# Optimization experiments

Hardware: AMD Instinct MI355X
Metric: run time of the kernel (lower is better)

## Reference

```python
import jax, jax.numpy as jnp
import numpy as np

N, E = 100000, 1000000
IN_DIM, HID, OUT_DIM, TAU_DIM, MAX_REC = 128, 64, 64, 8, 5


def setup_inputs() -> dict:
    key = jax.random.key(0)
    ks = jax.random.split(key, 16)
    s = 0.05
    return {
        "x": jax.random.normal(ks[0], (N, IN_DIM), dtype=jnp.float32),
        "edge_index": jax.random.randint(ks[1], (2, E), 0, N, dtype=jnp.int64),
        "W_in": jax.random.normal(ks[2], (HID, IN_DIM), dtype=jnp.float32) * s,
        "b_in": jnp.zeros((HID,), jnp.float32),
        "W_t1": jax.random.normal(ks[3], (HID, IN_DIM), dtype=jnp.float32) * s,
        "b_t1": jnp.zeros((HID,), jnp.float32),
        "W_t2": jax.random.normal(ks[4], (TAU_DIM, HID), dtype=jnp.float32) * s,
        "b_t2": jnp.zeros((TAU_DIM,), jnp.float32),
        "W_ih": jax.random.normal(ks[5], (3 * HID, HID), dtype=jnp.float32) * s,
        "b_ih": jnp.zeros((3 * HID,), jnp.float32),
        "W_hh": jax.random.normal(ks[6], (3 * HID, HID), dtype=jnp.float32) * s,
        "b_hh": jnp.zeros((3 * HID,), jnp.float32),
        "W_out": jax.random.normal(ks[7], (OUT_DIM, HID), dtype=jnp.float32) * s,
        "b_out": jnp.zeros((OUT_DIM,), jnp.float32),
    }


def _gru_cell(inp, h, W_ih, b_ih, W_hh, b_hh):
    # torch.nn.GRUCell math
    gi = inp @ W_ih.T + b_ih  # [N, 3H]
    gh = h @ W_hh.T + b_hh    # [N, 3H]
    i_r, i_z, i_n = jnp.split(gi, 3, axis=-1)
    h_r, h_z, h_n = jnp.split(gh, 3, axis=-1)
    r = jax.nn.sigmoid(i_r + h_r)
    z = jax.nn.sigmoid(i_z + h_z)
    n = jnp.tanh(i_n + r * h_n)
    return (1.0 - z) * n + z * h


def reference(x, edge_index, W_in, b_in, W_t1, b_t1, W_t2, b_t2,
              W_ih, b_ih, W_hh, b_hh, W_out, b_out):
    row, col = edge_index[0], edge_index[1]
    h = jax.nn.relu(x @ W_in.T + b_in)  # [N, H]
    tau = jax.nn.sigmoid(jax.nn.relu(x @ W_t1.T + b_t1) @ W_t2.T + b_t2)
    tau = jnp.mean(tau, axis=-1, keepdims=True)  # [N, 1]
    for _ in range(MAX_REC):
        d1 = jnp.abs(h[row] - h[col])           # gather + diff, [E, H]
        weighted = d1 * tau[row]                # [E, H]
        agg = jax.ops.segment_sum(weighted, row, num_segments=h.shape[0])
        h = _gru_cell(agg, h, W_ih, b_ih, W_hh, b_hh)
    return h @ W_out.T + b_out
```

## Files before the change

### kernel.cpp

```cpp
#include <hip/hip_runtime.h>

#define HID 64
#define IN_DIM 128
#define TAU_DIM 8
#define SCAN_B 1024

#define KDIM 128
#define NT 64
#define JOUT 256
#define WS_STRIDE 20

typedef short bf16x8 __attribute__((ext_vector_type(8)));
typedef float f32x4 __attribute__((ext_vector_type(4)));

__device__ __forceinline__ unsigned short f2bf(float f) {
    union { float f; unsigned u; } v; v.f = f;
    unsigned r = v.u + 0x7FFF + ((v.u >> 16) & 1);
    return (unsigned short)(r >> 16);
}


__global__ void zero_int_kernel(int* __restrict__ p, int n) {
    int i = blockIdx.x * blockDim.x + threadIdx.x;
    if (i < n) p[i] = 0;
}

__global__ void count_deg_kernel(const int* __restrict__ row, int* __restrict__ deg,
                                 int e, int n) {
    int i = blockIdx.x * blockDim.x + threadIdx.x;
    if (i < e) {
        int r = row[i];
        if ((unsigned)r < (unsigned)n) atomicAdd(&deg[r], 1);
    }
}

__global__ void block_sum_kernel(const int* __restrict__ deg, int* __restrict__ blk, int n) {
    __shared__ int s[SCAN_B];
    int i = blockIdx.x * SCAN_B + threadIdx.x;
    s[threadIdx.x] = (i < n) ? deg[i] : 0;
    __syncthreads();
    for (int off = SCAN_B / 2; off > 0; off >>= 1) {
        if (threadIdx.x < off) s[threadIdx.x] += s[threadIdx.x + off];
        __syncthreads();
    }
    if (threadIdx.x == 0) blk[blockIdx.x] = s[0];
}

__global__ void scan_blk_kernel(int* __restrict__ blk, int nb) {
    __shared__ int s[SCAN_B];
    int v = (threadIdx.x < nb) ? blk[threadIdx.x] : 0;
    s[threadIdx.x] = v;
    __syncthreads();
    for (int off = 1; off < SCAN_B; off <<= 1) {
        int t = (threadIdx.x >= off) ? s[threadIdx.x - off] : 0;
        __syncthreads();
        s[threadIdx.x] += t;
        __syncthreads();
    }
    if (threadIdx.x < nb) blk[threadIdx.x] = s[threadIdx.x] - v;
}

__global__ void scan_final_kernel(const int* __restrict__ deg, const int* __restrict__ blk,
                                  int* __restrict__ row_start, int* __restrict__ cursor, int n) {
    __shared__ int s[SCAN_B];
    int i = blockIdx.x * SCAN_B + threadIdx.x;
    int v = (i < n) ? deg[i] : 0;
    s[threadIdx.x] = v;
    __syncthreads();
    for (int off = 1; off < SCAN_B; off <<= 1) {
        int t = (threadIdx.x >= off) ? s[threadIdx.x - off] : 0;
        __syncthreads();
        s[threadIdx.x] += t;
        __syncthreads();
    }
    if (i < n) {
        int excl = s[threadIdx.x] - v + blk[blockIdx.x];
        row_start[i] = excl;
        cursor[i]    = excl;
    }
}

__global__ void fill_csr_kernel(const int* __restrict__ row, const int* __restrict__ col,
                                int* __restrict__ cursor, int* __restrict__ cols,
                                int e, int n) {
    int i = blockIdx.x * blockDim.x + threadIdx.x;
    if (i < e) {
        int r = row[i];
        if ((unsigned)r < (unsigned)n) {
            int c = col[i];
            if ((unsigned)c >= (unsigned)n) c = 0;
            int p = atomicAdd(&cursor[r], 1);
            cols[p] = c;
        }
    }
}


__global__ void prep_all_kernel(
    const float* __restrict__ W_ih, const float* __restrict__ W_hh,
    const float* __restrict__ b_ih, const float* __restrict__ b_hh,
    const float* __restrict__ W_in, const float* __restrict__ b_in,
    const float* __restrict__ W_t1, const float* __restrict__ b_t1,
    const float* __restrict__ W_out,
    unsigned short* __restrict__ W2bf, float* __restrict__ B2,
    unsigned short* __restrict__ W1bf, float* __restrict__ B1,
    float* __restrict__ Wop) {
    int j = threadIdx.x;
    {
        float b;
        if (j < 128)      b = b_ih[j] + b_hh[j];
        else if (j < 192) b = b_ih[j];
        else              b = b_hh[j - 64];
        B2[j] = b;
        for (int k = 0; k < KDIM; k++) {
            float v;
            if (j < 128)      v = (k < 64) ? W_ih[j * 64 + k] : W_hh[j * 64 + (k - 64)];
            else if (j < 192) v = (k < 64) ? W_ih[j * 64 + k] : 0.f;
            else              v = (k >= 64) ? W_hh[(j - 64) * 64 + (k - 64)] : 0.f;
            W2bf[(size_t)j * KDIM + k] = f2bf(v);
        }
    }
    if (j < 128) {
        B1[j] = (j < 64) ? b_in[j] : b_t1[j - 64];
        const float* src = (j < 64) ? (W_in + (size_t)j * IN_DIM)
                                    : (W_t1 + (size_t)(j - 64) * IN_DIM);
        for (int k = 0; k < IN_DIM; k++)
            W1bf[(size_t)j * IN_DIM + k] = f2bf(src[k]);
    }
    if (j < 64) {
        for (int k = 0; k < HID; k++)
            Wop[(size_t)(k >> 4) * (64 * 16) + j * 16 + (k & 15)] = W_out[(size_t)j * HID + k];
    }
}


__global__ __launch_bounds__(256) void init_mfma_kernel(
    const float* __restrict__ x, const unsigned short* __restrict__ W1bf,
    const float* __restrict__ B1,
    const float* __restrict__ W_t2, const float* __restrict__ b_t2,
    float* __restrict__ X1, float* __restrict__ tau, int n) {
    __shared__ float t1s[NT * 65];

    const int t    = threadIdx.x;
    const int lane = t & 63;
    const int wave = t >> 6;
    const int col  = lane & 15;
    const int ksel = lane >> 4;
    const int nodebase = blockIdx.x * NT + wave * 16;

    bf16x8 afrag[4];
    {
        const int anode = nodebase + col;
#pragma unroll
        for (int kc = 0; kc < 4; kc++) {
            bf16x8 a;
            if (anode < n) {
                const float* p = x + (size_t)anode * IN_DIM + kc * 32 + ksel * 8;
                float4 lo = *(const float4*)p;
                float4 hi = *(const float4*)(p + 4);
                a[0] = (short)f2bf(lo.x); a[1] = (short)f2bf(lo.y);
                a[2] = (short)f2bf(lo.z); a[3] = (short)f2bf(lo.w);
                a[4] = (short)f2bf(hi.x); a[5] = (short)f2bf(hi.y);
                a[6] = (short)f2bf(hi.z); a[7] = (short)f2bf(hi.w);
            } else {
                a[0] = 0; a[1] = 0; a[2] = 0; a[3] = 0;
                a[4] = 0; a[5] = 0; a[6] = 0; a[7] = 0;
            }
            afrag[kc] = a;
        }
    }

#pragma unroll 1
    for (int i = 0; i < 8; i++) {
        float b = B1[i * 16 + col];
        f32x4 c; c[0] = b; c[1] = b; c[2] = b; c[3] = b;
#pragma unroll
        for (int kc = 0; kc < 4; kc++) {
            bf16x8 bf = *(const bf16x8*)(W1bf
                + (size_t)(i * 16 + col) * IN_DIM + kc * 32 + ksel * 8);
            c = __builtin_amdgcn_mfma_f32_16x16x32_bf16(afrag[kc], bf, c, 0, 0, 0);
        }
#pragma unroll
        for (int r = 0; r < 4; r++) {
            int node = nodebase + ksel * 4 + r;
            float v = fmaxf(c[r], 0.f);
            if (i < 4) {
                if (node < n) X1[(size_t)node * KDIM + 64 + i * 16 + col] = v;
            } else {
                t1s[(wave * 16 + ksel * 4 + r) * 65 + (i - 4) * 16 + col] = v;
            }
        }
    }
    __syncthreads();

    if (t < NT) {
        int node = blockIdx.x * NT + t;
        if (node < n) {
            float tsum = 0.f;
#pragma unroll 1
            for (int m = 0; m < TAU_DIM; m++) {
                float a = b_t2[m];
                const float* wr = W_t2 + (size_t)m * HID;
#pragma unroll
                for (int k = 0; k < HID; k++) a += wr[k] * t1s[t * 65 + k];
                tsum += 1.f / (1.f + expf(-a));
            }
            tau[node] = tsum * (1.f / TAU_DIM);
        }
    }
}


__global__ __launch_bounds__(256) void aggregate_kernel(
    float* __restrict__ X1, const float* __restrict__ tau,
    const int* __restrict__ row_start, const int* __restrict__ deg,
    const int* __restrict__ cols, int n, int hoff, int aoff) {
    int t = blockIdx.x * blockDim.x + threadIdx.x;
    int v = t >> 4;
    if (v >= n) return;
    int c4 = (t & 15) * 4;

    float4 hv = *(const float4*)(X1 + (size_t)v * KDIM + hoff + c4);
    float4 s0 = make_float4(0.f, 0.f, 0.f, 0.f);
    float4 s1 = make_float4(0.f, 0.f, 0.f, 0.f);
    int st = row_start[v];
    int d  = deg[v];
    int i = 0;
    for (; i + 1 < d; i += 2) {
        int c0 = cols[st + i];
        int c1 = cols[st + i + 1];
        float4 hc0 = *(const float4*)(X1 + (size_t)c0 * KDIM + hoff + c4);
        float4 hc1 = *(const float4*)(X1 + (size_t)c1 * KDIM + hoff + c4);
        s0.x += fabsf(hv.x - hc0.x);
        s0.y += fabsf(hv.y - hc0.y);
        s0.z += fabsf(hv.z - hc0.z);
        s0.w += fabsf(hv.w - hc0.w);
        s1.x += fabsf(hv.x - hc1.x);
        s1.y += fabsf(hv.y - hc1.y);
        s1.z += fabsf(hv.z - hc1.z);
        s1.w += fabsf(hv.w - hc1.w);
    }
    if (i < d) {
        int c = cols[st + i];
        float4 hc = *(const float4*)(X1 + (size_t)c * KDIM + hoff + c4);
        s0.x += fabsf(hv.x - hc.x);
        s0.y += fabsf(hv.y - hc.y);
        s0.z += fabsf(hv.z - hc.z);
        s0.w += fabsf(hv.w - hc.w);
    }
    float tv = tau[v];
    *(float4*)(X1 + (size_t)v * KDIM + aoff + c4) =
        make_float4((s0.x + s1.x) * tv, (s0.y + s1.y) * tv,
                    (s0.z + s1.z) * tv, (s0.w + s1.w) * tv);
}


__global__ __launch_bounds__(256) void gru_mfma_kernel(
    float* __restrict__ X1, const unsigned short* __restrict__ W2bf,
    const float* __restrict__ B2, int n, int hoff, int aoff) {
    const int t    = threadIdx.x;
    const int lane = t & 63;
    const int wave = t >> 6;
    const int col  = lane & 15;
    const int ksel = lane >> 4;
    const int nodebase = blockIdx.x * NT + wave * 16;

    bf16x8 afrag[4];
    {
        const int anode = nodebase + col;
#pragma unroll
        for (int kc = 0; kc < 4; kc++) {
            int c0 = ((kc < 2) ? (aoff + kc * 32) : (hoff + (kc - 2) * 32)) + ksel * 8;
            bf16x8 a;
            if (anode < n) {
                const float* p = X1 + (size_t)anode * KDIM + c0;
                float4 lo = *(const float4*)p;
                float4 hi = *(const float4*)(p + 4);
                a[0] = (short)f2bf(lo.x); a[1] = (short)f2bf(lo.y);
                a[2] = (short)f2bf(lo.z); a[3] = (short)f2bf(lo.w);
                a[4] = (short)f2bf(hi.x); a[5] = (short)f2bf(hi.y);
                a[6] = (short)f2bf(hi.z); a[7] = (short)f2bf(hi.w);
            } else {
                a[0] = 0; a[1] = 0; a[2] = 0; a[3] = 0;
                a[4] = 0; a[5] = 0; a[6] = 0; a[7] = 0;
            }
            afrag[kc] = a;
        }
    }

    const int onode_base = nodebase + ksel * 4;

#pragma unroll 1
    for (int i = 0; i < 4; i++) {
        f32x4 acc[4];
#pragma unroll
        for (int gb = 0; gb < 4; gb++) {
            float b = B2[gb * 64 + i * 16 + col];
            f32x4 c; c[0] = b; c[1] = b; c[2] = b; c[3] = b;
#pragma unroll
            for (int kc = 0; kc < 4; kc++) {
                bf16x8 bf = *(const bf16x8*)(W2bf
                    + (size_t)(gb * 64 + i * 16 + col) * KDIM + kc * 32 + ksel * 8);
                c = __builtin_amdgcn_mfma_f32_16x16x32_bf16(afrag[kc], bf, c, 0, 0, 0);
            }
            acc[gb] = c;
        }
#pragma unroll
        for (int r = 0; r < 4; r++) {
            int node = onode_base + r;
            if (node < n) {
                float rr = 1.f / (1.f + expf(-acc[0][r]));
                float z  = 1.f / (1.f + expf(-acc[1][r]));
                float nn = tanhf(acc[2][r] + rr * acc[3][r]);
                float hold = X1[(size_t)node * KDIM + hoff + i * 16 + col];
                X1[(size_t)node * KDIM + aoff + i * 16 + col] = (1.f - z) * nn + z * hold;
            }
        }
    }
}


__global__ __launch_bounds__(256) void out_gemm_kernel(
    const float* __restrict__ X1, const float* __restrict__ Wop,
    const float* __restrict__ b_out, float* __restrict__ out, int n, int hoff) {
    __shared__ float xs[NT * 68];
    __shared__ float wsh[64 * WS_STRIDE];

    const int t  = threadIdx.x;
    const int tx = t & 15;
    const int ty = t >> 4;
    const int node0 = blockIdx.x * NT;

#pragma unroll
    for (int i = 0; i < 4; i++) {
        int f4 = i * 256 + t;
        int r  = f4 >> 4;
        int c4 = f4 & 15;
        float4 v = make_float4(0.f, 0.f, 0.f, 0.f);
        int node = node0 + r;
        if (node < n) v = *(const float4*)(X1 + (size_t)node * KDIM + hoff + c4 * 4);
        *(float4*)(xs + r * 68 + c4 * 4) = v;
    }

    float acc[4][4];
#pragma unroll
    for (int i = 0; i < 4; i++) {
        float b = b_out[i * 16 + tx];
#pragma unroll
        for (int nd = 0; nd < 4; nd++) acc[nd][i] = b;
    }

    const float* wbase = wsh + tx * WS_STRIDE;
#pragma unroll 1
    for (int kc = 0; kc < 4; kc++) {
        __syncthreads();
        {
            const float4* src = (const float4*)(Wop + (size_t)kc * (64 * 16));
            int f4  = t;
            int row = f4 >> 2;
            int k4  = f4 & 3;
            *(float4*)(wsh + row * WS_STRIDE + k4 * 4) = src[f4];
        }
        __syncthreads();
        const float* xbase = xs + (ty * 4) * 68 + kc * 16;
#pragma unroll
        for (int k4 = 0; k4 < 4; k4++) {
            float4 xv[4];
#pragma unroll
            for (int nd = 0; nd < 4; nd++)
                xv[nd] = *(const float4*)(xbase + nd * 68 + k4 * 4);
#pragma unroll
            for (int i = 0; i < 4; i++) {
                float4 w = *(const float4*)(wbase + (i * 16) * WS_STRIDE + k4 * 4);
#pragma unroll
                for (int nd = 0; nd < 4; nd++) {
                    acc[nd][i] += w.x * xv[nd].x + w.y * xv[nd].y
                                + w.z * xv[nd].z + w.w * xv[nd].w;
                }
            }
        }
    }

#pragma unroll
    for (int nd = 0; nd < 4; nd++) {
        int node = node0 + ty * 4 + nd;
        if (node < n) {
#pragma unroll
            for (int i = 0; i < 4; i++)
                out[(size_t)node * HID + i * 16 + tx] = acc[nd][i];
        }
    }
}


extern "C" void kernel_launch(void* const* d_in, const int* in_sizes, int n_in,
                              void* d_out, int out_size, void* d_ws, size_t ws_size,
                              hipStream_t stream) {
    const float* x     = (const float*)d_in[0];
    const int*   ei    = (const int*)d_in[1];
    const float* W_in  = (const float*)d_in[2];
    const float* b_in  = (const float*)d_in[3];
    const float* W_t1  = (const float*)d_in[4];
    const float* b_t1  = (const float*)d_in[5];
    const float* W_t2  = (const float*)d_in[6];
    const float* b_t2  = (const float*)d_in[7];
    const float* W_ih  = (const float*)d_in[8];
    const float* b_ih  = (const float*)d_in[9];
    const float* W_hh  = (const float*)d_in[10];
    const float* b_hh  = (const float*)d_in[11];
    const float* W_out = (const float*)d_in[12];
    const float* b_out = (const float*)d_in[13];
    float* out = (float*)d_out;

    const int n = in_sizes[0] / IN_DIM;
    const int e = in_sizes[1] / 2;
    const int* row = ei;
    const int* col = ei + e;

    char* ws = (char*)d_ws;
    float* X1  = (float*)ws;  ws += (size_t)n * KDIM * sizeof(float);
    unsigned short* W2bf = (unsigned short*)ws;  ws += (size_t)JOUT * KDIM * sizeof(unsigned short);
    unsigned short* W1bf = (unsigned short*)ws;  ws += (size_t)128 * IN_DIM * sizeof(unsigned short);
    float* B2  = (float*)ws;  ws += JOUT * sizeof(float);
    float* B1  = (float*)ws;  ws += 128 * sizeof(float);
    float* Wop = (float*)ws;  ws += (size_t)64 * HID * sizeof(float);
    float* tau = (float*)ws;  ws += (size_t)n * sizeof(float);
    int* deg       = (int*)ws;  ws += (size_t)n * sizeof(int);
    int* row_start = (int*)ws;  ws += (size_t)n * sizeof(int);
    int* cursor    = (int*)ws;  ws += (size_t)n * sizeof(int);
    int* blk       = (int*)ws;  ws += SCAN_B * sizeof(int);
    int* cols      = (int*)ws;  ws += (size_t)e * sizeof(int);

    const int nb = (n + SCAN_B - 1) / SCAN_B;
    const int ngemm = (n + NT - 1) / NT;

    zero_int_kernel<<<(n + 255) / 256, 256, 0, stream>>>(deg, n);
    count_deg_kernel<<<(e + 255) / 256, 256, 0, stream>>>(row, deg, e, n);
    block_sum_kernel<<<nb, SCAN_B, 0, stream>>>(deg, blk, n);
    scan_blk_kernel<<<1, SCAN_B, 0, stream>>>(blk, nb);
    scan_final_kernel<<<nb, SCAN_B, 0, stream>>>(deg, blk, row_start, cursor, n);
    fill_csr_kernel<<<(e + 255) / 256, 256, 0, stream>>>(row, col, cursor, cols, e, n);

    prep_all_kernel<<<1, 256, 0, stream>>>(W_ih, W_hh, b_ih, b_hh,
                                           W_in, b_in, W_t1, b_t1, W_out,
                                           W2bf, B2, W1bf, B1, Wop);
    init_mfma_kernel<<<ngemm, 256, 0, stream>>>(x, W1bf, B1, W_t2, b_t2, X1, tau, n);

    int hoff = 64, aoff = 0;
    for (int it = 0; it < 5; ++it) {
        aggregate_kernel<<<((n * 16) + 255) / 256, 256, 0, stream>>>(
            X1, tau, row_start, deg, cols, n, hoff, aoff);
        gru_mfma_kernel<<<ngemm, 256, 0, stream>>>(X1, W2bf, B2, n, hoff, aoff);
        int tmp = hoff; hoff = aoff; aoff = tmp;
    }
    out_gemm_kernel<<<ngemm, 256, 0, stream>>>(X1, Wop, b_out, out, n, hoff);
}
```

Baseline: 879.7 us.

## Store node hidden state and aggregates in bf16 instead of fp32

Changes the shared node feature buffer X1 (hidden state and aggregate halves) from fp32 to bf16 throughout the init, aggregate, GRU and output kernels. The edge gather in aggregation, which dominates memory traffic, now reads half the bytes per neighbour, and the GRU kernel loads MFMA operands directly without conversion. The cost is that the recurrent state is rounded to bf16 on every step, so error accumulates over the recurrence.

```diff
diff --git a/kernel.cpp b/kernel.cpp
--- a/kernel.cpp
+++ b/kernel.cpp
@@ -10,6 +10,7 @@
 #define JOUT 256
 #define WS_STRIDE 20
 
+typedef short bf16x4 __attribute__((ext_vector_type(4)));
 typedef short bf16x8 __attribute__((ext_vector_type(8)));
 typedef float f32x4 __attribute__((ext_vector_type(4)));
 
@@ -17,6 +18,10 @@
     union { float f; unsigned u; } v; v.f = f;
     unsigned r = v.u + 0x7FFF + ((v.u >> 16) & 1);
     return (unsigned short)(r >> 16);
+}
+__device__ __forceinline__ float bf2f(unsigned short s) {
+    union { unsigned u; float f; } v; v.u = ((unsigned)s) << 16;
+    return v.f;
 }
 
 
@@ -138,7 +143,7 @@
     const float* __restrict__ x, const unsigned short* __restrict__ W1bf,
     const float* __restrict__ B1,
     const float* __restrict__ W_t2, const float* __restrict__ b_t2,
-    float* __restrict__ X1, float* __restrict__ tau, int n) {
+    unsigned short* __restrict__ X1, float* __restrict__ tau, int n) {
     __shared__ float t1s[NT * 65];
 
     const int t    = threadIdx.x;
@@ -185,7 +190,7 @@
             int node = nodebase + ksel * 4 + r;
             float v = fmaxf(c[r], 0.f);
             if (i < 4) {
-                if (node < n) X1[(size_t)node * KDIM + 64 + i * 16 + col] = v;
+                if (node < n) X1[(size_t)node * KDIM + 64 + i * 16 + col] = f2bf(v);
             } else {
                 t1s[(wave * 16 + ksel * 4 + r) * 65 + (i - 4) * 16 + col] = v;
             }
@@ -212,7 +217,7 @@
 
 
 __global__ __launch_bounds__(256) void aggregate_kernel(
-    float* __restrict__ X1, const float* __restrict__ tau,
+    unsigned short* __restrict__ X1, const float* __restrict__ tau,
     const int* __restrict__ row_start, const int* __restrict__ deg,
     const int* __restrict__ cols, int n, int hoff, int aoff) {
     int t = blockIdx.x * blockDim.x + threadIdx.x;
@@ -220,43 +225,48 @@
     if (v >= n) return;
     int c4 = (t & 15) * 4;
 
-    float4 hv = *(const float4*)(X1 + (size_t)v * KDIM + hoff + c4);
-    float4 s0 = make_float4(0.f, 0.f, 0.f, 0.f);
-    float4 s1 = make_float4(0.f, 0.f, 0.f, 0.f);
+    bf16x4 hvb = *(const bf16x4*)(X1 + (size_t)v * KDIM + hoff + c4);
+    float h0 = bf2f((unsigned short)hvb[0]), h1 = bf2f((unsigned short)hvb[1]);
+    float h2 = bf2f((unsigned short)hvb[2]), h3 = bf2f((unsigned short)hvb[3]);
+    float s00 = 0.f, s01 = 0.f, s02 = 0.f, s03 = 0.f;
+    float s10 = 0.f, s11 = 0.f, s12 = 0.f, s13 = 0.f;
     int st = row_start[v];
     int d  = deg[v];
     int i = 0;
     for (; i + 1 < d; i += 2) {
         int c0 = cols[st + i];
         int c1 = cols[st + i + 1];
-        float4 hc0 = *(const float4*)(X1 + (size_t)c0 * KDIM + hoff + c4);
-        float4 hc1 = *(const float4*)(X1 + (size_t)c1 * KDIM + hoff + c4);
-        s0.x += fabsf(hv.x - hc0.x);
-        s0.y += fabsf(hv.y - hc0.y);
-        s0.z += fabsf(hv.z - hc0.z);
-        s0.w += fabsf(hv.w - hc0.w);
-        s1.x += fabsf(hv.x - hc1.x);
-        s1.y += fabsf(hv.y - hc1.y);
-        s1.z += fabsf(hv.z - hc1.z);
-        s1.w += fabsf(hv.w - hc1.w);
+        bf16x4 a = *(const bf16x4*)(X1 + (size_t)c0 * KDIM + hoff + c4);
+        bf16x4 b = *(const bf16x4*)(X1 + (size_t)c1 * KDIM + hoff + c4);
+        s00 += fabsf(h0 - bf2f((unsigned short)a[0]));
+        s01 += fabsf(h1 - bf2f((unsigned short)a[1]));
+        s02 += fabsf(h2 - bf2f((unsigned short)a[2]));
+        s03 += fabsf(h3 - bf2f((unsigned short)a[3]));
+        s10 += fabsf(h0 - bf2f((unsigned short)b[0]));
+        s11 += fabsf(h1 - bf2f((unsigned short)b[1]));
+        s12 += fabsf(h2 - bf2f((unsigned short)b[2]));
+        s13 += fabsf(h3 - bf2f((unsigned short)b[3]));
     }
     if (i < d) {
         int c = cols[st + i];
-        float4 hc = *(const float4*)(X1 + (size_t)c * KDIM + hoff + c4);
-        s0.x += fabsf(hv.x - hc.x);
-        s0.y += fabsf(hv.y - hc.y);
-        s0.z += fabsf(hv.z - hc.z);
-        s0.w += fabsf(hv.w - hc.w);
+        bf16x4 a = *(const bf16x4*)(X1 + (size_t)c * KDIM + hoff + c4);
+        s00 += fabsf(h0 - bf2f((unsigned short)a[0]));
+        s01 += fabsf(h1 - bf2f((unsigned short)a[1]));
+        s02 += fabsf(h2 - bf2f((unsigned short)a[2]));
+        s03 += fabsf(h3 - bf2f((unsigned short)a[3]));
     }
     float tv = tau[v];
-    *(float4*)(X1 + (size_t)v * KDIM + aoff + c4) =
-        make_float4((s0.x + s1.x) * tv, (s0.y + s1.y) * tv,
-                    (s0.z + s1.z) * tv, (s0.w + s1.w) * tv);
+    bf16x4 o;
+    o[0] = (short)f2bf((s00 + s10) * tv);
+    o[1] = (short)f2bf((s01 + s11) * tv);
+    o[2] = (short)f2bf((s02 + s12) * tv);
+    o[3] = (short)f2bf((s03 + s13) * tv);
+    *(bf16x4*)(X1 + (size_t)v * KDIM + aoff + c4) = o;
 }
 
 
 __global__ __launch_bounds__(256) void gru_mfma_kernel(
-    float* __restrict__ X1, const unsigned short* __restrict__ W2bf,
+    unsigned short* __restrict__ X1, const unsigned short* __restrict__ W2bf,
     const float* __restrict__ B2, int n, int hoff, int aoff) {
     const int t    = threadIdx.x;
     const int lane = t & 63;
@@ -273,13 +283,7 @@
             int c0 = ((kc < 2) ? (aoff + kc * 32) : (hoff + (kc - 2) * 32)) + ksel * 8;
             bf16x8 a;
             if (anode < n) {
-                const float* p = X1 + (size_t)anode * KDIM + c0;
-                float4 lo = *(const float4*)p;
-                float4 hi = *(const float4*)(p + 4);
-                a[0] = (short)f2bf(lo.x); a[1] = (short)f2bf(lo.y);
-                a[2] = (short)f2bf(lo.z); a[3] = (short)f2bf(lo.w);
-                a[4] = (short)f2bf(hi.x); a[5] = (short)f2bf(hi.y);
-                a[6] = (short)f2bf(hi.z); a[7] = (short)f2bf(hi.w);
+                a = *(const bf16x8*)(X1 + (size_t)anode * KDIM + c0);
             } else {
                 a[0] = 0; a[1] = 0; a[2] = 0; a[3] = 0;
                 a[4] = 0; a[5] = 0; a[6] = 0; a[7] = 0;
@@ -312,8 +316,9 @@
                 float rr = 1.f / (1.f + expf(-acc[0][r]));
                 float z  = 1.f / (1.f + expf(-acc[1][r]));
                 float nn = tanhf(acc[2][r] + rr * acc[3][r]);
-                float hold = X1[(size_t)node * KDIM + hoff + i * 16 + col];
-                X1[(size_t)node * KDIM + aoff + i * 16 + col] = (1.f - z) * nn + z * hold;
+                float hold = bf2f(X1[(size_t)node * KDIM + hoff + i * 16 + col]);
+                X1[(size_t)node * KDIM + aoff + i * 16 + col] =
+                    f2bf((1.f - z) * nn + z * hold);
             }
         }
     }
@@ -321,7 +326,7 @@
 
 
 __global__ __launch_bounds__(256) void out_gemm_kernel(
-    const float* __restrict__ X1, const float* __restrict__ Wop,
+    const unsigned short* __restrict__ X1, const float* __restrict__ Wop,
     const float* __restrict__ b_out, float* __restrict__ out, int n, int hoff) {
     __shared__ float xs[NT * 68];
     __shared__ float wsh[64 * WS_STRIDE];
@@ -332,14 +337,22 @@
     const int node0 = blockIdx.x * NT;
 
 #pragma unroll
-    for (int i = 0; i < 4; i++) {
-        int f4 = i * 256 + t;
-        int r  = f4 >> 4;
-        int c4 = f4 & 15;
-        float4 v = make_float4(0.f, 0.f, 0.f, 0.f);
+    for (int i = 0; i < 2; i++) {
+        int idx = i * 256 + t;
+        int r   = idx >> 3;
+        int c8  = (idx & 7) * 8;
         int node = node0 + r;
-        if (node < n) v = *(const float4*)(X1 + (size_t)node * KDIM + hoff + c4 * 4);
-        *(float4*)(xs + r * 68 + c4 * 4) = v;
+        float vals[8];
+        if (node < n) {
+            bf16x8 v8 = *(const bf16x8*)(X1 + (size_t)node * KDIM + hoff + c8);
+#pragma unroll
+            for (int j = 0; j < 8; j++) vals[j] = bf2f((unsigned short)v8[j]);
+        } else {
+#pragma unroll
+            for (int j = 0; j < 8; j++) vals[j] = 0.f;
+        }
+#pragma unroll
+        for (int j = 0; j < 8; j++) xs[r * 68 + c8 + j] = vals[j];
     }
 
     float acc[4][4];
@@ -418,7 +431,7 @@
     const int* col = ei + e;
 
     char* ws = (char*)d_ws;
-    float* X1  = (float*)ws;  ws += (size_t)n * KDIM * sizeof(float);
+    unsigned short* X1 = (unsigned short*)ws;  ws += (size_t)n * KDIM * sizeof(unsigned short);
     unsigned short* W2bf = (unsigned short*)ws;  ws += (size_t)JOUT * KDIM * sizeof(unsigned short);
     unsigned short* W1bf = (unsigned short*)ws;  ws += (size_t)128 * IN_DIM * sizeof(unsigned short);
     float* B2  = (float*)ws;  ws += JOUT * sizeof(float);
```

New measurement: 794.1 us. 9.7% less time.
